# Optimization experiments

Measured on AMD Instinct MI355X. Metric: run time of the kernel, lower is better.

The kernel has to match this reference:

```python
import jax, jax.numpy as jnp
import numpy as np

B, C, H, W = 32, 64, 64, 64
NUM_CODES = 1024
COMMITMENT_COST = 0.25


def setup_inputs() -> dict:
    key = jax.random.key(0)
    k1, k2 = jax.random.split(key)
    z = jax.random.normal(k1, (B, C, H, W), dtype=jnp.float32)
    # matches nn.Embedding init uniform_(-1/num_codes, 1/num_codes)
    codebook = jax.random.uniform(k2, (NUM_CODES, C), dtype=jnp.float32,
                                  minval=-1.0 / NUM_CODES, maxval=1.0 / NUM_CODES)
    return {"z": z, "codebook": codebook}


def reference(z, codebook):
    # b c h w -> b h w c
    zt = jnp.transpose(z, (0, 2, 3, 1))
    b, h, w, c = zt.shape
    z_flat = zt.reshape(-1, c)  # (N, c)

    # squared L2 distances to each code: ||z||^2 + ||e||^2 - 2 z.e
    d = (jnp.sum(z_flat * z_flat, axis=1, keepdims=True)
         + jnp.sum(codebook * codebook, axis=1)[None, :]
         - 2.0 * z_flat @ codebook.T)  # (N, K)
    indices = jnp.argmin(d, axis=1)  # (N,)

    z_q = codebook[indices].reshape(b, h, w, c)

    codebook_loss = jnp.mean((z_q - jax.lax.stop_gradient(zt)) ** 2)
    commitment_loss = jnp.mean((zt - jax.lax.stop_gradient(z_q)) ** 2)
    loss = codebook_loss + COMMITMENT_COST * commitment_loss

    # straight-through estimator
    z_q_st = zt + jax.lax.stop_gradient(z_q - zt)
    z_q_out = jnp.transpose(z_q_st, (0, 3, 1, 2))  # b h w c -> b c h w
    return z_q_out, loss, indices.reshape(b, h, w)
```

## Files before the change

kernel.cpp:

```cpp
#include <hip/hip_runtime.h>

#define CDIM 64
#define KCODES 1024
#define ZQ_ELEMS (32 * 64 * 64 * 64)
#define NROWS 131072
#define FLT_BIG 3.402823466e38f
#define RPB 128
#define NBLK (NROWS / RPB)
#define CSTRIDE 49
#define DELTA 5e-4f

#define WS_BSQ_OFF 16384
#define WS_E1_OFF  32768

#define B_OFF     0
#define FRAG_OFF  4096
#define E_OFF     20736
#define SKEY_OFF  4096
#define SK_RD_OFF 29184
#define SK_RK_OFF 29696
#define SU_BYTES  30208

typedef __bf16 bf16x8 __attribute__((ext_vector_type(8)));
typedef float  f32x4  __attribute__((ext_vector_type(4)));

__device__ __forceinline__ float pairwise_sq64(const float* v) {
    float r[8];
    #pragma unroll
    for (int j = 0; j < 8; ++j) r[j] = __fmul_rn(v[j], v[j]);
    #pragma unroll
    for (int m = 1; m < 8; ++m) {
        #pragma unroll
        for (int j = 0; j < 8; ++j)
            r[j] = __fadd_rn(r[j], __fmul_rn(v[8 * m + j], v[8 * m + j]));
    }
    return __fadd_rn(__fadd_rn(__fadd_rn(r[0], r[1]), __fadd_rn(r[2], r[3])),
                     __fadd_rn(__fadd_rn(r[4], r[5]), __fadd_rn(r[6], r[7])));
}

__global__ __launch_bounds__(256) void vq_prep(const float* __restrict__ cb,
                                               float* __restrict__ Bsq,
                                               __bf16* __restrict__ e1) {
    const int k = blockIdx.x * 256 + threadIdx.x;
    const float* __restrict__ ck = cb + k * CDIM;
    float v[CDIM];
    #pragma unroll
    for (int q = 0; q < 16; ++q) {
        float4 t = ((const float4*)ck)[q];
        v[4 * q + 0] = t.x; v[4 * q + 1] = t.y; v[4 * q + 2] = t.z; v[4 * q + 3] = t.w;
    }
    Bsq[k] = pairwise_sq64(v);

    const int t = k >> 4, kin = k & 15;
    bf16x8* F1 = (bf16x8*)e1;
    #pragma unroll
    for (int ks = 0; ks < 2; ++ks) {
        #pragma unroll
        for (int g = 0; g < 4; ++g) {
            bf16x8 a;
            #pragma unroll
            for (int i = 0; i < 8; ++i) a[i] = (__bf16)v[ks * 32 + 8 * g + i];
            F1[(t * 2 + ks) * 64 + ((g << 4) | kin)] = a;
        }
    }
}

#define INS(s, j, accv, Bv, code0) \
    { \
        const float vv = __fmaf_rn(-2.f, (accv), (Bv)); \
        const float kk = __int_as_float((__float_as_int(vv) & 0xFFFFFC00) | (code0)); \
        const float o0 = K0[s][j], o1 = K1[s][j], o2 = K2[s][j]; \
        K0[s][j] = fminf(o0, kk); \
        K1[s][j] = __builtin_amdgcn_fmed3f(o0, o1, kk); \
        K2[s][j] = __builtin_amdgcn_fmed3f(o1, o2, kk); \
    }

#define TILE_COMPUTE(Ea, Eb, code0) \
    { \
        const float Bv = sB[code0]; \
        f32x4 a0 = __builtin_amdgcn_mfma_f32_16x16x32_bf16(zh00, Ea, zero, 0, 0, 0); \
        a0       = __builtin_amdgcn_mfma_f32_16x16x32_bf16(zh01, Eb, a0, 0, 0, 0); \
        f32x4 a1 = __builtin_amdgcn_mfma_f32_16x16x32_bf16(zh10, Ea, zero, 0, 0, 0); \
        a1       = __builtin_amdgcn_mfma_f32_16x16x32_bf16(zh11, Eb, a1, 0, 0, 0); \
        INS(0, 0, a0[0], Bv, code0) INS(0, 1, a0[1], Bv, code0) \
        INS(0, 2, a0[2], Bv, code0) INS(0, 3, a0[3], Bv, code0) \
        INS(1, 0, a1[0], Bv, code0) INS(1, 1, a1[1], Bv, code0) \
        INS(1, 2, a1[2], Bv, code0) INS(1, 3, a1[3], Bv, code0) \
    }

__global__ __launch_bounds__(256, 4) void vq_main(const float* __restrict__ z,
                                                  const float* __restrict__ cb,
                                                  const float* __restrict__ Bsq,
                                                  const __bf16* __restrict__ e1,
                                                  float* __restrict__ zq_out,
                                                  float* __restrict__ idx_out,
                                                  double* __restrict__ part) {
    __shared__ __align__(16) unsigned char sU[SU_BYTES];
    __shared__ double sP2[2];
    float* __restrict__ sB = (float*)(sU + B_OFF);

    const int tid = threadIdx.x;
    const int n0 = blockIdx.x * RPB;
    const int b = n0 >> 12;
    const int hw0 = n0 & 4095;
    const float* __restrict__ zb = z + ((size_t)b << 18) + hw0;

    for (int k = tid; k < KCODES; k += 256) sB[k] = Bsq[k];

    {
        bf16x8* __restrict__ zfw = (bf16x8*)(sU + FRAG_OFF);
        const int r = tid & 127;
        const int h = tid >> 7;
        const int w = r >> 5, s = (r >> 4) & 1, li = r & 15;
        #pragma unroll
        for (int g = 0; g < 4; ++g) {
            bf16x8 hi;
            #pragma unroll
            for (int i = 0; i < 8; ++i) {
                const float fv = zb[((size_t)(32 * h + 8 * g + i) << 12) + r];
                hi[i] = (__bf16)fv;
            }
            zfw[(w * 4 + s * 2 + h) * 65 + ((g << 4) | li)] = hi;
        }
        *(float4*)(sU + E_OFF + tid * 16) =
            *(const float4*)((const unsigned char*)e1 + tid * 16);
    }
    __syncthreads();

    const int lane = tid & 63, w = tid >> 6;
    const int g = lane >> 4, li = lane & 15;

    const bf16x8* __restrict__ zf = (const bf16x8*)(sU + FRAG_OFF);
    const bf16x8 zh00 = zf[(w * 4 + 0) * 65 + lane];
    const bf16x8 zh01 = zf[(w * 4 + 1) * 65 + lane];
    const bf16x8 zh10 = zf[(w * 4 + 2) * 65 + lane];
    const bf16x8 zh11 = zf[(w * 4 + 3) * 65 + lane];

    float K0[2][4], K1[2][4], K2[2][4];
    #pragma unroll
    for (int s = 0; s < 2; ++s)
        #pragma unroll
        for (int j = 0; j < 4; ++j) { K0[s][j] = FLT_BIG; K1[s][j] = FLT_BIG; K2[s][j] = FLT_BIG; }

    const f32x4 zero = {0.f, 0.f, 0.f, 0.f};

    for (int c = 0; c < 32; ++c) {
        const float4 vstage =
            *(const float4*)((const unsigned char*)e1 + (c + 1) * 4096 + tid * 16);
        const bf16x8* __restrict__ buf = (const bf16x8*)(sU + E_OFF + (c & 1) * 4096);
        const int cb0 = c * 32 + li;
        TILE_COMPUTE(buf[lane],       buf[64 + lane],  cb0)
        *(float4*)(sU + E_OFF + ((c + 1) & 1) * 4096 + tid * 16) = vstage;
        TILE_COMPUTE(buf[128 + lane], buf[192 + lane], cb0 + 16)
        __syncthreads();
    }

    float* __restrict__ sKey = (float*)(sU + SKEY_OFF);
    float* __restrict__ sRd = (float*)(sU + SK_RD_OFF);
    int*   __restrict__ sRk = (int*)(sU + SK_RK_OFF);
    #pragma unroll
    for (int s = 0; s < 2; ++s) {
        #pragma unroll
        for (int j = 0; j < 4; ++j) {
            const int row = 32 * w + 16 * s + 4 * g + j;
            const int base = row * CSTRIDE + li * 3;
            sKey[base + 0] = K0[s][j];
            sKey[base + 1] = K1[s][j];
            sKey[base + 2] = K2[s][j];
        }
    }
    __syncthreads();

    {
        const int r = tid & 127;
        const int half = tid >> 7;
        const int n = n0 + r;

        float gmin = FLT_BIG;
        #pragma unroll
        for (int s2 = 0; s2 < 48; ++s2) gmin = fminf(gmin, sKey[r * CSTRIDE + s2]);
        const float thr = gmin + DELTA;

        float zrow[CDIM];
        const float* __restrict__ zp = zb + r;
        #pragma unroll
        for (int c = 0; c < CDIM; ++c) zrow[c] = zp[(size_t)c << 12];
        const float A = pairwise_sq64(zrow);

        float bd = FLT_BIG;
        int bk = 1 << 30;
        const int sbeg = half * 24;
        for (int s2 = sbeg; s2 < sbeg + 24; ++s2) {
            const float kv = sKey[r * CSTRIDE + s2];
            if (kv <= thr) {
                const int k = __float_as_int(kv) & 0x3FF;
                const float4* __restrict__ ek = (const float4*)(cb + (size_t)k * CDIM);
                float m = 0.f;
                #pragma unroll
                for (int q = 0; q < 16; ++q) {
                    float4 e = ek[q];
                    m = __fmaf_rn(zrow[4 * q + 0], e.x, m);
                    m = __fmaf_rn(zrow[4 * q + 1], e.y, m);
                    m = __fmaf_rn(zrow[4 * q + 2], e.z, m);
                    m = __fmaf_rn(zrow[4 * q + 3], e.w, m);
                }
                const float d = __fsub_rn(__fadd_rn(A, sB[k]), __fadd_rn(m, m));
                if (d < bd || (d == bd && k < bk)) { bd = d; bk = k; }
            }
        }

        if (half == 1) { sRd[r] = bd; sRk[r] = bk; }
        __syncthreads();

        if (tid < RPB) {
            const float d1 = sRd[r];
            const int   k1 = sRk[r];
            if (d1 < bd || (d1 == bd && k1 < bk)) { bd = d1; bk = k1; }

            idx_out[n] = (float)bk;

            const float4* __restrict__ cq = (const float4*)(cb + (size_t)bk * CDIM);
            float* __restrict__ zo = zq_out + ((size_t)b << 18) + hw0 + r;
            float lsum = 0.f;
            #pragma unroll
            for (int q = 0; q < 16; ++q) {
                float4 qv = cq[q];
                zo[(size_t)(4 * q + 0) << 12] = qv.x;
                zo[(size_t)(4 * q + 1) << 12] = qv.y;
                zo[(size_t)(4 * q + 2) << 12] = qv.z;
                zo[(size_t)(4 * q + 3) << 12] = qv.w;
                lsum = fmaf(qv.x - zrow[4 * q + 0], qv.x - zrow[4 * q + 0], lsum);
                lsum = fmaf(qv.y - zrow[4 * q + 1], qv.y - zrow[4 * q + 1], lsum);
                lsum = fmaf(qv.z - zrow[4 * q + 2], qv.z - zrow[4 * q + 2], lsum);
                lsum = fmaf(qv.w - zrow[4 * q + 3], qv.w - zrow[4 * q + 3], lsum);
            }

            double ls = (double)lsum;
            for (int off = 32; off > 0; off >>= 1) ls += __shfl_down(ls, off, 64);
            if ((tid & 63) == 0) sP2[tid >> 6] = ls;
        }
    }
    __syncthreads();
    if (tid == 0) part[blockIdx.x] = sP2[0] + sP2[1];
}

__global__ void vq_finalize(const double* __restrict__ part, float* __restrict__ loss_out) {
    __shared__ double s[16];
    const int tid = threadIdx.x;
    double v = part[tid];
    for (int off = 32; off > 0; off >>= 1) v += __shfl_down(v, off, 64);
    if ((tid & 63) == 0) s[tid >> 6] = v;
    __syncthreads();
    if (tid == 0) {
        double t = 0.0;
        #pragma unroll
        for (int i = 0; i < 16; ++i) t += s[i];
        *loss_out = (float)(1.25 * t / (double)ZQ_ELEMS);
    }
}

extern "C" void kernel_launch(void* const* d_in, const int* in_sizes, int n_in,
                              void* d_out, int out_size, void* d_ws, size_t ws_size,
                              hipStream_t stream) {
    const float* z  = (const float*)d_in[0];
    const float* cb = (const float*)d_in[1];
    float* out  = (float*)d_out;
    float* zq   = out;
    float* loss = out + ZQ_ELEMS;
    float* idx  = out + ZQ_ELEMS + 1;
    char* ws = (char*)d_ws;
    double* part = (double*)ws;
    float* Bsq   = (float*)(ws + WS_BSQ_OFF);
    __bf16* e1   = (__bf16*)(ws + WS_E1_OFF);

    vq_prep<<<4, 256, 0, stream>>>(cb, Bsq, e1);
    vq_main<<<NBLK, 256, 0, stream>>>(z, cb, Bsq, e1, zq, idx, part);
    vq_finalize<<<1, 1024, 0, stream>>>(part, loss);
}
```

Baseline: 71.10 us.

## Deepen codebook staging to four LDS buffers and halve barriers per chunk

The codebook streaming loop moves from a double buffer to a four-slot LDS ring. Two 4 KB chunks are processed per iteration, and the global loads are issued two iterations ahead in registers. Barriers drop from one per chunk to one per pair, using a raw s_waitcnt plus s_barrier to hide global latency and cut sync overhead. The cost is more LDS per block, which may lower occupancy, and extra register pressure. The global loads at indices c0+4 and c0+5 also run past the codebook on the last iterations, as the old loop already did.

```diff
diff --git a/kernel.cpp b/kernel.cpp
--- a/kernel.cpp
+++ b/kernel.cpp
@@ -19,7 +19,7 @@
 #define SKEY_OFF  4096
 #define SK_RD_OFF 29184
 #define SK_RK_OFF 29696
-#define SU_BYTES  30208
+#define SU_BYTES  37120
 
 typedef __bf16 bf16x8 __attribute__((ext_vector_type(8)));
 typedef float  f32x4  __attribute__((ext_vector_type(4)));
@@ -124,7 +124,12 @@
         }
         *(float4*)(sU + E_OFF + tid * 16) =
             *(const float4*)((const unsigned char*)e1 + tid * 16);
-    }
+        *(float4*)(sU + E_OFF + 4096 + tid * 16) =
+            *(const float4*)((const unsigned char*)e1 + 4096 + tid * 16);
+    }
+
+    float4 vP0 = *(const float4*)((const unsigned char*)e1 + 2 * 4096 + tid * 16);
+    float4 vP1 = *(const float4*)((const unsigned char*)e1 + 3 * 4096 + tid * 16);
     __syncthreads();
 
     const int lane = tid & 63, w = tid >> 6;
@@ -144,16 +149,32 @@
 
     const f32x4 zero = {0.f, 0.f, 0.f, 0.f};
 
-    for (int c = 0; c < 32; ++c) {
-        const float4 vstage =
-            *(const float4*)((const unsigned char*)e1 + (c + 1) * 4096 + tid * 16);
-        const bf16x8* __restrict__ buf = (const bf16x8*)(sU + E_OFF + (c & 1) * 4096);
-        const int cb0 = c * 32 + li;
-        TILE_COMPUTE(buf[lane],       buf[64 + lane],  cb0)
-        *(float4*)(sU + E_OFF + ((c + 1) & 1) * 4096 + tid * 16) = vstage;
-        TILE_COMPUTE(buf[128 + lane], buf[192 + lane], cb0 + 16)
-        __syncthreads();
-    }
+    for (int i = 0; i < 16; ++i) {
+        const int c0 = 2 * i;
+        const float4 vN0 =
+            *(const float4*)((const unsigned char*)e1 + (c0 + 4) * 4096 + tid * 16);
+        const float4 vN1 =
+            *(const float4*)((const unsigned char*)e1 + (c0 + 5) * 4096 + tid * 16);
+        *(float4*)(sU + E_OFF + ((c0 + 2) & 3) * 4096 + tid * 16) = vP0;
+        *(float4*)(sU + E_OFF + ((c0 + 3) & 3) * 4096 + tid * 16) = vP1;
+
+        const bf16x8* __restrict__ bufA = (const bf16x8*)(sU + E_OFF + (c0 & 3) * 4096);
+        const bf16x8* __restrict__ bufB = (const bf16x8*)(sU + E_OFF + ((c0 + 1) & 3) * 4096);
+        const int cbA = c0 * 32 + li;
+        const int cbB = (c0 + 1) * 32 + li;
+        TILE_COMPUTE(bufA[lane],       bufA[64 + lane],  cbA)
+        TILE_COMPUTE(bufA[128 + lane], bufA[192 + lane], cbA + 16)
+        TILE_COMPUTE(bufB[lane],       bufB[64 + lane],  cbB)
+        TILE_COMPUTE(bufB[128 + lane], bufB[192 + lane], cbB + 16)
+
+        vP0 = vN0;
+        vP1 = vN1;
+        asm volatile("s_waitcnt lgkmcnt(0)" ::: "memory");
+        __builtin_amdgcn_s_barrier();
+        __builtin_amdgcn_sched_barrier(0);
+    }
+
+    __syncthreads();
 
     float* __restrict__ sKey = (float*)(sU + SKEY_OFF);
     float* __restrict__ sRd = (float*)(sU + SK_RD_OFF);
```

After: 67.55 us (median of 2 runs). 1.05x faster.
